# Optimization experiments

Measured on AMD Instinct MI355X. Metric: run time of the kernel, lower is better.

The kernel has to match this reference:

```python
import jax, jax.numpy as jnp
import numpy as np

N_NODES = 1024
CHANNELS = [1, 64, 128]
DENSE = [196608, 256]
SAMPLE_NUMBER = 50


def _glorot(key, shape):
    fan_in, fan_out = shape[0], shape[-1]
    s = jnp.sqrt(6.0 / (fan_in + fan_out))
    return jax.random.uniform(key, shape, jnp.float32, -s, s)


def setup_inputs() -> dict:
    key = jax.random.key(0)
    ks = jax.random.split(key, 20)
    T, B = 16, 64
    inp = {
        "xs_seq": jax.random.normal(ks[0], (T, B, N_NODES, CHANNELS[0]), jnp.float32),
        "adj": jax.random.uniform(ks[1], (N_NODES, N_NODES), jnp.float32) / N_NODES,
    }
    # GCGRU params per layer: gates z, r, candidate n over concat([x, h])
    ki = 2
    for li in range(len(CHANNELS) - 1):
        cin, cout = CHANNELS[li], CHANNELS[li + 1]
        for g in ("z", "r", "n"):
            inp[f"W{g}{li}"] = _glorot(ks[ki], (cin + cout, cout)); ki += 1
            inp[f"b{g}{li}"] = jnp.zeros((cout,), jnp.float32)
    inp["W_mu"] = _glorot(ks[ki], (DENSE[0], DENSE[1])); ki += 1
    inp["b_mu"] = jnp.zeros((DENSE[1],), jnp.float32)
    inp["W_lv"] = _glorot(ks[ki], (DENSE[0], DENSE[1])); ki += 1
    inp["b_lv"] = jnp.zeros((DENSE[1],), jnp.float32)
    return inp


def _gcgru(xs, adj, Wz, bz, Wr, br, Wn, bn, cout):
    # xs: [T, B, N, cin]; graph-conv GRU over time via scan
    T, B, N, _ = xs.shape
    h0 = jnp.zeros((B, N, cout), xs.dtype)

    def gconv(a, x, W, b):  # adj @ x @ W + b
        return jnp.einsum("ij,bjc,cd->bid", a, x, W) + b

    def step(h, x):
        xh = jnp.concatenate([x, h], axis=-1)
        z = jax.nn.sigmoid(gconv(adj, xh, Wz, bz))
        r = jax.nn.sigmoid(gconv(adj, xh, Wr, br))
        xrh = jnp.concatenate([x, r * h], axis=-1)
        n = jnp.tanh(gconv(adj, xrh, Wn, bn))
        h_new = (1.0 - z) * h + z * n
        return h_new, h_new

    _, hs = jax.lax.scan(step, h0, xs)
    return hs  # [T, B, N, cout]


def _forward(xs_seq, adj, Wz0, bz0, Wr0, br0, Wn0, bn0,
             Wz1, bz1, Wr1, br1, Wn1, bn1, W_mu, b_mu, W_lv, b_lv, eps):
    h1 = _gcgru(xs_seq, adj, Wz0, bz0, Wr0, br0, Wn0, bn0, CHANNELS[1])
    h2 = _gcgru(h1, adj, Wz1, bz1, Wr1, br1, Wn1, bn1, CHANNELS[2])
    xs = jnp.concatenate([h1[-1], h2[-1]], axis=2)  # [B, N, C1+C2]
    B = xs.shape[0]
    xs = xs.reshape(B, -1)  # [B, N*(C1+C2)]
    mu = jax.nn.sigmoid(xs @ W_mu + b_mu)
    logvar = jax.nn.sigmoid(xs @ W_lv + b_lv)
    std = jnp.exp(0.5 * logvar)
    z = mu + eps * std
    return z, mu, logvar


def reference(xs_seq, adj, Wz0, bz0, Wr0, br0, Wn0, bn0,
              Wz1, bz1, Wr1, br1, Wn1, bn1, W_mu, b_mu, W_lv, b_lv):
    B = xs_seq.shape[1]
    ekey = jax.random.fold_in(jax.random.key(0), 1234)
    eps = jax.random.normal(ekey, (SAMPLE_NUMBER, B, DENSE[1]), jnp.float32).mean(0)
    return _forward(xs_seq, adj, Wz0, bz0, Wr0, br0, Wn0, bn0,
                    Wz1, bz1, Wr1, br1, Wn1, bn1, W_mu, b_mu, W_lv, b_lv, eps)
```

## Files before the change

### kernel.cpp

```cpp
#include <hip/hip_runtime.h>
#include <math.h>

#define EPS_MODE 0

typedef unsigned short u16;
typedef short bf16x8 __attribute__((ext_vector_type(8)));
typedef float f32x4 __attribute__((ext_vector_type(4)));
typedef u16 u16x4 __attribute__((ext_vector_type(4)));
typedef u16 u16x8 __attribute__((ext_vector_type(8)));

static constexpr int T = 16;
static constexpr size_t MF = 1u << 20;
static constexpr int DKCH = 256;
static constexpr int DKCHUNK = 196608 / DKCH;

__device__ __forceinline__ u16 f2bf(float f) {
  unsigned u = __float_as_uint(f);
  unsigned r = (u + 0x7fffu + ((u >> 16) & 1u)) >> 16;
  return (u16)r;
}
__device__ __forceinline__ float bf2f(u16 h) {
  return __uint_as_float(((unsigned)h) << 16);
}
__device__ __forceinline__ void gload16(const void* g, void* l) {
  __builtin_amdgcn_global_load_lds(
      (const __attribute__((address_space(1))) void*)g,
      (__attribute__((address_space(3))) void*)l, 16, 0, 0);
}
__device__ __forceinline__ float sigm(float x) { return 1.f / (1.f + expf(-x)); }

__global__ __launch_bounds__(256) void cast_bf16(const float* __restrict__ in,
                                                 u16* __restrict__ out, int n) {
  int i = (blockIdx.x * 256 + threadIdx.x) * 4;
  if (i < n) {
    float4 v = *reinterpret_cast<const float4*>(&in[i]);
    out[i + 0] = f2bf(v.x); out[i + 1] = f2bf(v.y);
    out[i + 2] = f2bf(v.z); out[i + 3] = f2bf(v.w);
  }
}

__global__ __launch_bounds__(256) void prep_wt(const float* __restrict__ Wz0, const float* __restrict__ Wr0,
                                               const float* __restrict__ Wn0, const float* __restrict__ Wz1,
                                               const float* __restrict__ Wr1, const float* __restrict__ Wn1,
                                               u16* __restrict__ WzrT0, u16* __restrict__ WnT0,
                                               u16* __restrict__ WzrT1, u16* __restrict__ WnT1) {
  int seg = blockIdx.y;
  int idx = blockIdx.x * 256 + threadIdx.x;
  if (seg == 0) {
    if (idx < 128 * 64) {
      int j = idx >> 6, k = idx & 63;
      float v = (j < 64) ? Wz0[(k + 1) * 64 + j] : Wr0[(k + 1) * 64 + (j - 64)];
      WzrT0[idx] = f2bf(v);
    }
  } else if (seg == 1) {
    if (idx < 64 * 64) {
      int j = idx >> 6, k = idx & 63;
      WnT0[idx] = f2bf(Wn0[(k + 1) * 64 + j]);
    }
  } else if (seg == 2) {
    if (idx < 256 * 192) {
      int j = idx / 192, k = idx % 192;
      float v = (j < 128) ? Wz1[k * 128 + j] : Wr1[k * 128 + (j - 128)];
      WzrT1[idx] = f2bf(v);
    }
  } else {
    if (idx < 128 * 192) {
      int j = idx / 192, k = idx % 192;
      WnT1[idx] = f2bf(Wn1[k * 128 + j]);
    }
  }
}

template <int EPI, int LOGC, int MFR>
__global__ __launch_bounds__(256) void adj_mfma(const u16* __restrict__ A,
                                                const u16* __restrict__ BT,
                                                void* __restrict__ OUT) {
  constexpr int MT = MFR * 32;
  __shared__ __align__(16) char lds[(MFR + 4) * 4096];
  int tid = threadIdx.x;
  int w = tid >> 6, lane = tid & 63;
  int row0 = blockIdx.y * MT, col0 = blockIdx.x * 128;
  int wm = w >> 1, wn = w & 1;
  f32x4 acc[MFR][4] = {};
  for (int k0 = 0; k0 < 1024; k0 += 64) {
#pragma unroll
    for (int q = 0; q < MFR; ++q) {
      int row = q * 32 + w * 8 + (lane >> 3);
      gload16(A + (size_t)(row0 + row) * 1024 + k0 + (lane & 7) * 8,
              lds + q * 4096 + w * 1024);
    }
#pragma unroll
    for (int q = 0; q < 4; ++q) {
      int row = q * 32 + w * 8 + (lane >> 3);
      gload16(BT + (size_t)(col0 + row) * 1024 + k0 + (lane & 7) * 8,
              lds + MFR * 4096 + q * 4096 + w * 1024);
    }
    __syncthreads();
#pragma unroll
    for (int kk = 0; kk < 2; ++kk) {
      bf16x8 a[MFR], bb[4];
#pragma unroll
      for (int m = 0; m < MFR; ++m)
        a[m] = *(const bf16x8*)(lds + (wm * (MFR * 16) + m * 16 + (lane & 15)) * 128 + kk * 64 + (lane >> 4) * 16);
#pragma unroll
      for (int n = 0; n < 4; ++n)
        bb[n] = *(const bf16x8*)(lds + MFR * 4096 + (wn * 64 + n * 16 + (lane & 15)) * 128 + kk * 64 + (lane >> 4) * 16);
#pragma unroll
      for (int m = 0; m < MFR; ++m)
#pragma unroll
        for (int n = 0; n < 4; ++n)
          acc[m][n] = __builtin_amdgcn_mfma_f32_16x16x32_bf16(a[m], bb[n], acc[m][n], 0, 0, 0);
    }
    __syncthreads();
  }
  if (EPI == 1) {
    float* O = (float*)OUT;
#pragma unroll
    for (int m = 0; m < MFR; ++m)
#pragma unroll
      for (int n = 0; n < 4; ++n) {
        int col = col0 + wn * 64 + n * 16 + (lane & 15);
        int t = col >> 6, bbx = col & 63;
        int row = row0 + wm * (MFR * 16) + m * 16 + ((lane >> 4) << 2);
        *(float4*)&O[((size_t)t << 16) + ((size_t)bbx << 10) + row] = *(float4*)&acc[m][n];
      }
  } else {
    u16* O = (u16*)OUT;
    constexpr int C = 1 << LOGC;
#pragma unroll
    for (int m = 0; m < MFR; ++m)
#pragma unroll
      for (int n = 0; n < 4; ++n) {
        int col = col0 + wn * 64 + n * 16 + (lane & 15);
        int bbx = col >> LOGC, c = col & (C - 1);
#pragma unroll
        for (int j = 0; j < 4; ++j) {
          int row = row0 + wm * (MFR * 16) + m * 16 + ((lane >> 4) << 2) + j;
          O[(((size_t)bbx << 10) + row) * C + c] = f2bf(acc[m][n][j]);
        }
      }
  }
}

template <int C, int RK1, int MFR>
__global__ __launch_bounds__(256) void adj_ngate(
    const u16* __restrict__ A, const u16* __restrict__ BT,
    const u16* __restrict__ WnT, const float* __restrict__ bias,
    const float* __restrict__ axv, const float* __restrict__ wx,
    const u16* __restrict__ AH1, const u16* __restrict__ zT,
    u16* __restrict__ hT) {
  constexpr int LOGC = (C == 64) ? 6 : 7;
  constexpr int KW = (C == 64) ? 64 : 192;
  constexpr int KKAN = C / 32;
  constexpr int MT = MFR * 32;
  constexpr int STG = (MFR + 4) * 4096;
  constexpr int ANBYTES = MT * 136 * 2;
  constexpr int LDSZ = STG > ANBYTES ? STG : ANBYTES;
  __shared__ __align__(16) char lds[LDSZ];
  int tid = threadIdx.x;
  int w = tid >> 6, lane = tid & 63;
  int row0 = blockIdx.y * MT, col0 = blockIdx.x * 128;
  int wm = w >> 1, wn = w & 1;
  f32x4 acc[MFR][4] = {};
  for (int k0 = 0; k0 < 1024; k0 += 64) {
#pragma unroll
    for (int q = 0; q < MFR; ++q) {
      int row = q * 32 + w * 8 + (lane >> 3);
      gload16(A + (size_t)(row0 + row) * 1024 + k0 + (lane & 7) * 8,
              lds + q * 4096 + w * 1024);
    }
#pragma unroll
    for (int q = 0; q < 4; ++q) {
      int row = q * 32 + w * 8 + (lane >> 3);
      gload16(BT + (size_t)(col0 + row) * 1024 + k0 + (lane & 7) * 8,
              lds + MFR * 4096 + q * 4096 + w * 1024);
    }
    __syncthreads();
#pragma unroll
    for (int kk = 0; kk < 2; ++kk) {
      bf16x8 a[MFR], bb[4];
#pragma unroll
      for (int m = 0; m < MFR; ++m)
        a[m] = *(const bf16x8*)(lds + (wm * (MFR * 16) + m * 16 + (lane & 15)) * 128 + kk * 64 + (lane >> 4) * 16);
#pragma unroll
      for (int n = 0; n < 4; ++n)
        bb[n] = *(const bf16x8*)(lds + MFR * 4096 + (wn * 64 + n * 16 + (lane & 15)) * 128 + kk * 64 + (lane >> 4) * 16);
#pragma unroll
      for (int m = 0; m < MFR; ++m)
#pragma unroll
        for (int n = 0; n < 4; ++n)
          acc[m][n] = __builtin_amdgcn_mfma_f32_16x16x32_bf16(a[m], bb[n], acc[m][n], 0, 0, 0);
    }
    __syncthreads();
  }
  u16* ANt = (u16*)lds;
#pragma unroll
  for (int m = 0; m < MFR; ++m)
#pragma unroll
    for (int n = 0; n < 4; ++n) {
      int cl = wn * 64 + n * 16 + (lane & 15);
      int rl = wm * (MFR * 16) + m * 16 + ((lane >> 4) << 2);
#pragma unroll
      for (int j = 0; j < 4; ++j)
        ANt[(rl + j) * 136 + cl] = f2bf(acc[m][n][j]);
    }
  __syncthreads();
  int wrow = w >> 1, half = w & 1;
  int arow0 = wrow * (MFR * 16);
  int b0 = col0 >> LOGC;
  int out0 = (C == 64) ? 0 : half * 64;
  int kbase = (C == 64) ? half * 64 : 0;
  int b_eff = (C == 64) ? (b0 + half) : b0;
  constexpr int WOFF = (C == 64) ? 0 : 64;
  f32x4 acc2[MFR][4] = {};
#pragma unroll
  for (int kk = 0; kk < KKAN; ++kk) {
    bf16x8 a[MFR], bb[4];
    int ka = kbase + kk * 32 + (lane >> 4) * 8;
#pragma unroll
    for (int m = 0; m < MFR; ++m)
      a[m] = *(const bf16x8*)&ANt[(arow0 + m * 16 + (lane & 15)) * 136 + ka];
#pragma unroll
    for (int n = 0; n < 4; ++n)
      bb[n] = *(const bf16x8*)&WnT[(size_t)(out0 + n * 16 + (lane & 15)) * KW + WOFF + kk * 32 + (lane >> 4) * 8];
#pragma unroll
    for (int m = 0; m < MFR; ++m)
#pragma unroll
      for (int n = 0; n < 4; ++n)
        acc2[m][n] = __builtin_amdgcn_mfma_f32_16x16x32_bf16(a[m], bb[n], acc2[m][n], 0, 0, 0);
  }
  if (C == 128) {
#pragma unroll
    for (int kk = 0; kk < 2; ++kk) {
      bf16x8 a[MFR], bb[4];
#pragma unroll
      for (int m = 0; m < MFR; ++m)
        a[m] = *(const bf16x8*)&AH1[(((size_t)b0 << 10) + row0 + arow0 + m * 16 + (lane & 15)) * 64 + kk * 32 + (lane >> 4) * 8];
#pragma unroll
      for (int n = 0; n < 4; ++n)
        bb[n] = *(const bf16x8*)&WnT[(size_t)(out0 + n * 16 + (lane & 15)) * 192 + kk * 32 + (lane >> 4) * 8];
#pragma unroll
      for (int m = 0; m < MFR; ++m)
#pragma unroll
        for (int n = 0; n < 4; ++n)
          acc2[m][n] = __builtin_amdgcn_mfma_f32_16x16x32_bf16(a[m], bb[n], acc2[m][n], 0, 0, 0);
    }
  }
#pragma unroll
  for (int m = 0; m < MFR; ++m) {
    float ax4[4];
    if (RK1) {
      float4 v = *(const float4*)&axv[((size_t)b_eff << 10) + row0 + arow0 + m * 16 + ((lane >> 4) << 2)];
      ax4[0] = v.x; ax4[1] = v.y; ax4[2] = v.z; ax4[3] = v.w;
    }
#pragma unroll
    for (int n = 0; n < 4; ++n) {
      int cp = out0 + n * 16 + (lane & 15);
      int grow = arow0 + m * 16 + ((lane >> 4) << 2);
      size_t idx = (((size_t)b_eff << LOGC) + cp) * 1024 + row0 + grow;
      u16x4 zv = *(const u16x4*)&zT[idx];
      u16x4 hv = *(const u16x4*)&hT[idx];
      u16x4 pk;
#pragma unroll
      for (int j = 0; j < 4; ++j) {
        float g = acc2[m][n][j] + bias[cp];
        if (RK1) g += ax4[j] * wx[cp];
        float nv = tanhf(g);
        float z = bf2f(zv[j]), ho = bf2f(hv[j]);
        pk[j] = f2bf((1.f - z) * ho + z * nv);
      }
      *(u16x4*)&hT[idx] = pk;
    }
  }
}

template <int WM, int WN, int C, int NK1, int NK, int RK1>
__global__ __launch_bounds__(256) void gate_zr(
    const u16* __restrict__ A1, const u16* __restrict__ A2,
    const u16* __restrict__ WT, const float* __restrict__ bz,
    const float* __restrict__ br, const float* __restrict__ axv,
    const float* __restrict__ wxz, const float* __restrict__ wxr,
    const u16* __restrict__ hT, u16* __restrict__ zTo, u16* __restrict__ rhTo) {
  constexpr int MT = WM * 64, NT = WN * 64, K = NK * 64;
  constexpr int NB = 1024 / MT;
  __shared__ __align__(16) char lds[MT * 128 + NT * 128];
  int tid = threadIdx.x;
  int w = tid >> 6, lane = tid & 63;
  int by = blockIdx.x;
  int b = by / NB, n0 = (by % NB) * MT;
  size_t row0 = ((size_t)b << 10) + n0;
  int wm = w / WN, wn = w % WN;
  f32x4 acc[4][4] = {};
  for (int s = 0; s < NK; ++s) {
    const u16* As; int astr, koff;
    if (s < NK1) { As = A1; astr = 64; koff = s * 64; }
    else         { As = A2; astr = 128; koff = (s - NK1) * 64; }
#pragma unroll
    for (int q = 0; q < MT / 32; ++q) {
      int row = q * 32 + w * 8 + (lane >> 3);
      gload16(As + (row0 + row) * astr + koff + (lane & 7) * 8,
              lds + q * 4096 + w * 1024);
    }
#pragma unroll
    for (int q = 0; q < NT / 32; ++q) {
      int row = q * 32 + w * 8 + (lane >> 3);
      gload16(WT + (size_t)row * K + s * 64 + (lane & 7) * 8,
              lds + MT * 128 + q * 4096 + w * 1024);
    }
    __syncthreads();
#pragma unroll
    for (int kk = 0; kk < 2; ++kk) {
      bf16x8 a[4], bb[4];
#pragma unroll
      for (int m = 0; m < 4; ++m)
        a[m] = *(const bf16x8*)(lds + (wm * 64 + m * 16 + (lane & 15)) * 128 + kk * 64 + (lane >> 4) * 16);
#pragma unroll
      for (int n = 0; n < 4; ++n)
        bb[n] = *(const bf16x8*)(lds + MT * 128 + (wn * 64 + n * 16 + (lane & 15)) * 128 + kk * 64 + (lane >> 4) * 16);
#pragma unroll
      for (int m = 0; m < 4; ++m)
#pragma unroll
        for (int n = 0; n < 4; ++n)
          acc[m][n] = __builtin_amdgcn_mfma_f32_16x16x32_bf16(a[m], bb[n], acc[m][n], 0, 0, 0);
    }
    __syncthreads();
  }
#pragma unroll
  for (int m = 0; m < 4; ++m) {
    float ax4[4];
    if (RK1) {
      float4 v = *(const float4*)&axv[row0 + wm * 64 + m * 16 + ((lane >> 4) << 2)];
      ax4[0] = v.x; ax4[1] = v.y; ax4[2] = v.z; ax4[3] = v.w;
    }
#pragma unroll
    for (int n = 0; n < 4; ++n) {
      int cp = wn * 64 + n * 16 + (lane & 15);
      bool iz = cp < C;
      int c = iz ? cp : cp - C;
      int rl = wm * 64 + m * 16 + ((lane >> 4) << 2);
      size_t idx = (((size_t)b * C + c) << 10) + n0 + rl;
      u16x4 hv;
      if (!iz) hv = *(const u16x4*)&hT[idx];
      u16x4 pk;
#pragma unroll
      for (int j = 0; j < 4; ++j) {
        float g = acc[m][n][j] + (iz ? bz : br)[c];
        if (RK1) g += ax4[j] * (iz ? wxz : wxr)[c];
        float sg = sigm(g);
        pk[j] = iz ? f2bf(sg) : f2bf(sg * bf2f(hv[j]));
      }
      *(u16x4*)&(iz ? zTo : rhTo)[idx] = pk;
    }
  }
}

__global__ __launch_bounds__(256) void ah1_zr(
    const u16* __restrict__ adjB, const u16* __restrict__ h1T,
    const u16* __restrict__ AH2, const u16* __restrict__ h2T,
    const u16* __restrict__ WzrT1, const float* __restrict__ bz1, const float* __restrict__ br1,
    const u16* __restrict__ WzrT0, const float* __restrict__ bz0, const float* __restrict__ br0,
    const float* __restrict__ AXt1, const float* __restrict__ wz0x, const float* __restrict__ wr0x,
    u16* __restrict__ AH1, u16* __restrict__ z1T, u16* __restrict__ rh1T,
    u16* __restrict__ z0T, u16* __restrict__ rh0T, int do_zr0) {
  __shared__ __align__(16) char lds[24576];
  int tid = threadIdx.x, w = tid >> 6, lane = tid & 63;
  int row0 = blockIdx.y * 64, col0 = blockIdx.x * 128;
  int b0 = col0 >> 6;
  int wm = w >> 1, wn = w & 1;
  f32x4 acc[2][4] = {};
  for (int k0 = 0; k0 < 1024; k0 += 64) {
#pragma unroll
    for (int q = 0; q < 2; ++q) {
      int row = q * 32 + w * 8 + (lane >> 3);
      gload16(adjB + (size_t)(row0 + row) * 1024 + k0 + (lane & 7) * 8,
              lds + q * 4096 + w * 1024);
    }
#pragma unroll
    for (int q = 0; q < 4; ++q) {
      int row = q * 32 + w * 8 + (lane >> 3);
      gload16(h1T + (size_t)(col0 + row) * 1024 + k0 + (lane & 7) * 8,
              lds + 8192 + q * 4096 + w * 1024);
    }
    __syncthreads();
#pragma unroll
    for (int kk = 0; kk < 2; ++kk) {
      bf16x8 a[2], bb[4];
#pragma unroll
      for (int m = 0; m < 2; ++m)
        a[m] = *(const bf16x8*)(lds + (wm * 32 + m * 16 + (lane & 15)) * 128 + kk * 64 + (lane >> 4) * 16);
#pragma unroll
      for (int n = 0; n < 4; ++n)
        bb[n] = *(const bf16x8*)(lds + 8192 + (wn * 64 + n * 16 + (lane & 15)) * 128 + kk * 64 + (lane >> 4) * 16);
#pragma unroll
      for (int m = 0; m < 2; ++m)
#pragma unroll
        for (int n = 0; n < 4; ++n)
          acc[m][n] = __builtin_amdgcn_mfma_f32_16x16x32_bf16(a[m], bb[n], acc[m][n], 0, 0, 0);
    }
    __syncthreads();
  }
  u16* ANt = (u16*)lds;
#pragma unroll
  for (int m = 0; m < 2; ++m)
#pragma unroll
    for (int n = 0; n < 4; ++n) {
      int col = wn * 64 + n * 16 + (lane & 15);
      int bl = col >> 6, c = col & 63;
      int rl = wm * 32 + m * 16 + ((lane >> 4) << 2);
#pragma unroll
      for (int j = 0; j < 4; ++j) {
        u16 v = f2bf(acc[m][n][j]);
        AH1[(((size_t)(b0 + bl) << 10) + row0 + rl + j) * 64 + c] = v;
        ANt[(bl * 64 + rl + j) * 72 + c] = v;
      }
    }
  __syncthreads();
  int b = b0 + wm;
#pragma unroll
  for (int hz = 0; hz < 2; ++hz) {
    f32x4 g1[4][4] = {};
#pragma unroll
    for (int kk = 0; kk < 2; ++kk) {
      bf16x8 a[4], bb[4];
#pragma unroll
      for (int m = 0; m < 4; ++m)
        a[m] = *(const bf16x8*)&ANt[(wm * 64 + m * 16 + (lane & 15)) * 72 + kk * 32 + (lane >> 4) * 8];
#pragma unroll
      for (int n = 0; n < 4; ++n) {
        int out = hz * 128 + wn * 64 + n * 16 + (lane & 15);
        bb[n] = *(const bf16x8*)&WzrT1[(size_t)out * 192 + kk * 32 + (lane >> 4) * 8];
      }
#pragma unroll
      for (int m = 0; m < 4; ++m)
#pragma unroll
        for (int n = 0; n < 4; ++n)
          g1[m][n] = __builtin_amdgcn_mfma_f32_16x16x32_bf16(a[m], bb[n], g1[m][n], 0, 0, 0);
    }
#pragma unroll
    for (int kk = 0; kk < 4; ++kk) {
      bf16x8 a[4], bb[4];
#pragma unroll
      for (int m = 0; m < 4; ++m) {
        int gn = row0 + m * 16 + (lane & 15);
        a[m] = *(const bf16x8*)&AH2[(((size_t)b << 10) + gn) * 128 + kk * 32 + (lane >> 4) * 8];
      }
#pragma unroll
      for (int n = 0; n < 4; ++n) {
        int out = hz * 128 + wn * 64 + n * 16 + (lane & 15);
        bb[n] = *(const bf16x8*)&WzrT1[(size_t)out * 192 + 64 + kk * 32 + (lane >> 4) * 8];
      }
#pragma unroll
      for (int m = 0; m < 4; ++m)
#pragma unroll
        for (int n = 0; n < 4; ++n)
          g1[m][n] = __builtin_amdgcn_mfma_f32_16x16x32_bf16(a[m], bb[n], g1[m][n], 0, 0, 0);
    }
#pragma unroll
    for (int m = 0; m < 4; ++m)
#pragma unroll
      for (int n = 0; n < 4; ++n) {
        int outq = hz * 128 + wn * 64 + n * 16 + (lane & 15);
        bool iz = outq < 128;
        int c = iz ? outq : outq - 128;
        int gr = m * 16 + ((lane >> 4) << 2);
        size_t idx = (((size_t)b * 128 + c) << 10) + row0 + gr;
        u16x4 hv;
        if (!iz) hv = *(const u16x4*)&h2T[idx];
        u16x4 pk;
#pragma unroll
        for (int j = 0; j < 4; ++j) {
          float g = g1[m][n][j] + (iz ? bz1 : br1)[c];
          float sg = sigm(g);
          pk[j] = iz ? f2bf(sg) : f2bf(sg * bf2f(hv[j]));
        }
        *(u16x4*)&(iz ? z1T : rh1T)[idx] = pk;
      }
  }
  if (do_zr0) {
    f32x4 g0[4][4] = {};
#pragma unroll
    for (int kk = 0; kk < 2; ++kk) {
      bf16x8 a[4], bb[4];
#pragma unroll
      for (int m = 0; m < 4; ++m)
        a[m] = *(const bf16x8*)&ANt[(wm * 64 + m * 16 + (lane & 15)) * 72 + kk * 32 + (lane >> 4) * 8];
#pragma unroll
      for (int n = 0; n < 4; ++n) {
        int out = wn * 64 + n * 16 + (lane & 15);
        bb[n] = *(const bf16x8*)&WzrT0[(size_t)out * 64 + kk * 32 + (lane >> 4) * 8];
      }
#pragma unroll
      for (int m = 0; m < 4; ++m)
#pragma unroll
        for (int n = 0; n < 4; ++n)
          g0[m][n] = __builtin_amdgcn_mfma_f32_16x16x32_bf16(a[m], bb[n], g0[m][n], 0, 0, 0);
    }
#pragma unroll
    for (int m = 0; m < 4; ++m) {
      int gr0 = m * 16 + ((lane >> 4) << 2);
      float4 av = *(const float4*)&AXt1[((size_t)b << 10) + row0 + gr0];
      float ax4[4] = {av.x, av.y, av.z, av.w};
#pragma unroll
      for (int n = 0; n < 4; ++n) {
        int out = wn * 64 + n * 16 + (lane & 15);
        bool iz = out < 64;
        int c = out & 63;
        size_t idx = (((size_t)b * 64 + c) << 10) + row0 + gr0;
        u16x4 hv;
        if (!iz) hv = *(const u16x4*)&h1T[idx];
        u16x4 pk;
#pragma unroll
        for (int j = 0; j < 4; ++j) {
          float g = g0[m][n][j] + (iz ? bz0 : br0)[c] + ax4[j] * (iz ? wz0x : wr0x)[c];
          float sg = sigm(g);
          pk[j] = iz ? f2bf(sg) : f2bf(sg * bf2f(hv[j]));
        }
        *(u16x4*)&(iz ? z0T : rh0T)[idx] = pk;
      }
    }
  }
}

__global__ __launch_bounds__(256) void transpose_x(const u16* __restrict__ h1T,
                                                   const u16* __restrict__ h2T,
                                                   u16* __restrict__ X) {
  int b = blockIdx.x;
  int n0 = blockIdx.y * 128;
  __shared__ u16 tile[192][136];
  int tid = threadIdx.x;
#pragma unroll
  for (int i = 0; i < 12; ++i) {
    int id = tid + i * 256;
    int c = id >> 4, g = id & 15;
    u16x8 v;
    if (c < 64) v = *(const u16x8*)&h1T[(((size_t)b << 6) + c) * 1024 + n0 + g * 8];
    else        v = *(const u16x8*)&h2T[(((size_t)b << 7) + (c - 64)) * 1024 + n0 + g * 8];
    *(u16x8*)&tile[c][g * 8] = v;
  }
  __syncthreads();
#pragma unroll
  for (int i = 0; i < 12; ++i) {
    int id = tid + i * 256;
    int n = id / 24, g = id % 24;
    u16x8 v;
#pragma unroll
    for (int j = 0; j < 8; ++j) v[j] = tile[g * 8 + j][n];
    *(u16x8*)&X[(size_t)b * 196608 + (size_t)(n0 + n) * 192 + g * 8] = v;
  }
}

__global__ __launch_bounds__(256) void dense_mfma3(const u16* __restrict__ X,
                                                   const float* __restrict__ Wmu,
                                                   const float* __restrict__ Wlv,
                                                   float* __restrict__ P) {
  __shared__ __align__(16) char lds[8192 + 128 * 70 * 2];
  u16* Bs = (u16*)(lds + 8192);
  int tid = threadIdx.x, w = tid >> 6, lane = tid & 63;
  int o0 = blockIdx.x * 128;
  int ch = blockIdx.y, mat = blockIdx.z;
  const float* W = mat ? Wlv : Wmu;
  int kb = ch * DKCHUNK;
  int oL = tid & 63;
  f32x4 acc[4][2] = {};
  for (int s = 0; s < DKCHUNK / 64; ++s) {
    int kg = kb + s * 64;
#pragma unroll
    for (int q = 0; q < 2; ++q) {
      int row = q * 32 + w * 8 + (lane >> 3);
      gload16(X + (size_t)row * 196608 + kg + (lane & 7) * 8,
              lds + q * 4096 + w * 1024);
    }
#pragma unroll
    for (int og = 0; og < 2; ++og) {
      int o = og * 64 + oL;
      float v[16];
#pragma unroll
      for (int kk = 0; kk < 16; ++kk)
        v[kk] = W[(size_t)(kg + w * 16 + kk) * 256 + o0 + o];
      u16x8 p0, p1;
#pragma unroll
      for (int j = 0; j < 8; ++j) p0[j] = f2bf(v[j]);
#pragma unroll
      for (int j = 0; j < 8; ++j) p1[j] = f2bf(v[8 + j]);
      *(u16x8*)&Bs[o * 70 + w * 16] = p0;
      *(u16x8*)&Bs[o * 70 + w * 16 + 8] = p1;
    }
    __syncthreads();
#pragma unroll
    for (int kk = 0; kk < 2; ++kk) {
      bf16x8 a[4], bb[2];
#pragma unroll
      for (int m = 0; m < 4; ++m)
        a[m] = *(const bf16x8*)(lds + (m * 16 + (lane & 15)) * 128 + kk * 64 + (lane >> 4) * 16);
#pragma unroll
      for (int n = 0; n < 2; ++n) {
        int o = w * 32 + n * 16 + (lane & 15);
        bb[n] = *(const bf16x8*)&Bs[o * 70 + kk * 32 + (lane >> 4) * 8];
      }
#pragma unroll
      for (int m = 0; m < 4; ++m)
#pragma unroll
        for (int n = 0; n < 2; ++n)
          acc[m][n] = __builtin_amdgcn_mfma_f32_16x16x32_bf16(a[m], bb[n], acc[m][n], 0, 0, 0);
    }
    __syncthreads();
  }
#pragma unroll
  for (int m = 0; m < 4; ++m)
#pragma unroll
    for (int n = 0; n < 2; ++n) {
      int o = o0 + w * 32 + n * 16 + (lane & 15);
#pragma unroll
      for (int j = 0; j < 4; ++j) {
        int row = m * 16 + ((lane >> 4) << 2) + j;
        P[(((size_t)mat * DKCH + ch) * 64 + row) * 256 + o] = acc[m][n][j];
      }
    }
}

__device__ __forceinline__ unsigned rotl32(unsigned v, int s) {
  return (v << s) | (v >> (32 - s));
}
__device__ void threefry(unsigned k0, unsigned k1, unsigned x0, unsigned x1,
                         unsigned& o0, unsigned& o1) {
  unsigned ks2 = k0 ^ k1 ^ 0x1BD11BDAu;
  unsigned a = x0 + k0, b = x1 + k1;
#define TF_RND(rot) { a += b; b = rotl32(b, rot); b ^= a; }
  TF_RND(13) TF_RND(15) TF_RND(26) TF_RND(6)
  a += k1; b += ks2 + 1u;
  TF_RND(17) TF_RND(29) TF_RND(16) TF_RND(24)
  a += ks2; b += k0 + 2u;
  TF_RND(13) TF_RND(15) TF_RND(26) TF_RND(6)
  a += k0; b += k1 + 3u;
  TF_RND(17) TF_RND(29) TF_RND(16) TF_RND(24)
  a += k1; b += ks2 + 4u;
  TF_RND(13) TF_RND(15) TF_RND(26) TF_RND(6)
  a += ks2; b += k0 + 5u;
#undef TF_RND
  o0 = a; o1 = b;
}

__device__ float u32_to_normal(unsigned bits) {
  unsigned fb = (bits >> 9) | 0x3F800000u;
  float f = __uint_as_float(fb) - 1.0f;
  const float lo = -0.99999994f;
  float u = f * 2.0f + lo;
  u = fmaxf(lo, u);
  float w = -log1pf(-u * u);
  float p;
  if (w < 5.0f) {
    w -= 2.5f;
    p = 2.81022636e-08f;
    p = fmaf(p, w, 3.43273939e-07f);
    p = fmaf(p, w, -3.5233877e-06f);
    p = fmaf(p, w, -4.39150654e-06f);
    p = fmaf(p, w, 0.00021858087f);
    p = fmaf(p, w, -0.00125372503f);
    p = fmaf(p, w, -0.00417768164f);
    p = fmaf(p, w, 0.246640727f);
    p = fmaf(p, w, 1.50140941f);
  } else {
    w = sqrtf(w) - 3.0f;
    p = -0.000200214257f;
    p = fmaf(p, w, 0.000100950558f);
    p = fmaf(p, w, 0.00134934322f);
    p = fmaf(p, w, -0.00367342844f);
    p = fmaf(p, w, 0.00573950773f);
    p = fmaf(p, w, -0.0076224613f);
    p = fmaf(p, w, 0.00943887047f);
    p = fmaf(p, w, 1.00167406f);
    p = fmaf(p, w, 2.83297682f);
  }
  return 1.41421354f * (p * u);
}

__global__ __launch_bounds__(256) void eps_kernel(float* __restrict__ eps) {
  int b = blockIdx.x;
  int o = threadIdx.x;
  unsigned k0, k1;
  threefry(0u, 0u, 0u, 1234u, k0, k1);
  float s = 0.f;
  for (int smp = 0; smp < 50; ++smp) {
    unsigned idx = ((unsigned)smp * 64u + (unsigned)b) * 256u + (unsigned)o;
    unsigned o0, o1, bits;
#if EPS_MODE == 0
    threefry(k0, k1, 0u, idx, o0, o1);
    bits = o0 ^ o1;
#else
    unsigned pp = idx % 409600u, half = idx / 409600u;
    threefry(k0, k1, pp, pp + 409600u, o0, o1);
    bits = half ? o1 : o0;
#endif
    s += u32_to_normal(bits);
  }
  eps[b * 256 + o] = s / 50.0f;
}

__global__ __launch_bounds__(256) void final_kernel(const float* __restrict__ P,
                                                    const float* __restrict__ bmu,
                                                    const float* __restrict__ blv,
                                                    const float* __restrict__ eps,
                                                    float* __restrict__ out) {
  int b = blockIdx.x, o = threadIdx.x;
  float smu = 0.f, slv = 0.f;
  for (int ch = 0; ch < DKCH; ++ch) {
    smu += P[(((size_t)0 * DKCH + ch) * 64 + b) * 256 + o];
    slv += P[(((size_t)1 * DKCH + ch) * 64 + b) * 256 + o];
  }
  float mu = sigm(smu + bmu[o]);
  float lv = sigm(slv + blv[o]);
  float z = mu + eps[b * 256 + o] * expf(0.5f * lv);
  out[b * 256 + o] = z;
  out[16384 + b * 256 + o] = mu;
  out[32768 + b * 256 + o] = lv;
}

extern "C" void kernel_launch(void* const* d_in, const int* in_sizes, int n_in,
                              void* d_out, int out_size, void* d_ws, size_t ws_size,
                              hipStream_t stream) {
  (void)in_sizes; (void)n_in; (void)out_size; (void)ws_size;
  const float* xs  = (const float*)d_in[0];
  const float* adj = (const float*)d_in[1];
  const float* Wz0 = (const float*)d_in[2];  const float* bz0 = (const float*)d_in[3];
  const float* Wr0 = (const float*)d_in[4];  const float* br0 = (const float*)d_in[5];
  const float* Wn0 = (const float*)d_in[6];  const float* bn0 = (const float*)d_in[7];
  const float* Wz1 = (const float*)d_in[8];  const float* bz1 = (const float*)d_in[9];
  const float* Wr1 = (const float*)d_in[10]; const float* br1 = (const float*)d_in[11];
  const float* Wn1 = (const float*)d_in[12]; const float* bn1 = (const float*)d_in[13];
  const float* Wmu = (const float*)d_in[14]; const float* bmu = (const float*)d_in[15];
  const float* Wlv = (const float*)d_in[16]; const float* blv = (const float*)d_in[17];

  float* ws = (float*)d_ws;
  u16*  adjB  = (u16*)(ws);
  u16*  xsB   = (u16*)(ws + MF / 2);
  float* AXv  = ws + 1 * MF;
  u16*  h1T   = (u16*)(ws + 2 * MF);
  u16*  h2T   = (u16*)(ws + 4 * MF);
  u16*  z0T   = (u16*)(ws + 8 * MF);
  u16*  z1T   = (u16*)(ws + 10 * MF);
  u16*  rh0T  = (u16*)(ws + 14 * MF);
  u16*  rh1T  = (u16*)(ws + 16 * MF);
  u16*  AH1   = (u16*)(ws + 20 * MF);
  u16*  AH2   = (u16*)(ws + 22 * MF);
  u16*  WTb   = (u16*)(ws + 26 * MF);
  u16*  X     = (u16*)(ws + 8 * MF);
  float* P    = ws + 16 * MF;
  float* EPS  = ws + 24 * MF;

  u16* WzrT0 = WTb;
  u16* WnT0  = WTb + 8192;
  u16* WzrT1 = WTb + 12288;
  u16* WnT1  = WTb + 61440;

  hipMemsetAsync(ws + 2 * MF, 0, 6 * MF * sizeof(float), stream);
  hipMemsetAsync(ws + 20 * MF, 0, 6 * MF * sizeof(float), stream);

  cast_bf16<<<1024, 256, 0, stream>>>(adj, adjB, 1 << 20);
  cast_bf16<<<1024, 256, 0, stream>>>(xs, xsB, 1 << 20);
  prep_wt<<<dim3(192, 4), 256, 0, stream>>>(Wz0, Wr0, Wn0, Wz1, Wr1, Wn1,
                                            WzrT0, WnT0, WzrT1, WnT1);

  adj_mfma<1, 0, 4><<<dim3(8, 8), 256, 0, stream>>>(adjB, xsB, AXv);

  gate_zr<2, 2, 64, 1, 1, 1><<<512, 256, 0, stream>>>(
      AH1, nullptr, WzrT0, bz0, br0, AXv, Wz0, Wr0, h1T, z0T, rh0T);

  for (int t = 0; t < T; ++t) {
    const float* AXt = AXv + (size_t)t * 65536;
    const float* AXn = AXv + (size_t)((t + 1 < T) ? t + 1 : t) * 65536;
    adj_ngate<64, 1, 2><<<dim3(32, 16), 256, 0, stream>>>(
        adjB, rh0T, WnT0, bn0, AXt, Wn0, nullptr, z0T, h1T);
    ah1_zr<<<dim3(32, 16), 256, 0, stream>>>(
        adjB, h1T, AH2, h2T, WzrT1, bz1, br1, WzrT0, bz0, br0,
        AXn, Wz0, Wr0, AH1, z1T, rh1T, z0T, rh0T, (t + 1 < T) ? 1 : 0);
    adj_ngate<128, 0, 4><<<dim3(64, 8), 256, 0, stream>>>(
        adjB, rh1T, WnT1, bn1, nullptr, nullptr, AH1, z1T, h2T);
    if (t + 1 < T)
      adj_mfma<0, 7, 4><<<dim3(64, 8), 256, 0, stream>>>(adjB, h2T, AH2);
  }

  transpose_x<<<dim3(64, 8), 256, 0, stream>>>(h1T, h2T, X);
  dense_mfma3<<<dim3(2, DKCH, 2), 256, 0, stream>>>(X, Wmu, Wlv, P);
  eps_kernel<<<64, 256, 0, stream>>>(EPS);
  final_kernel<<<64, 256, 0, stream>>>(P, bmu, blv, EPS, (float*)d_out);
}
```

Measured before the change: 2.784 ms.

## Fuse next-step layer-0 n-gate with layer-1 adj matmul into one launch

Turns the adj_mfma and adj_ngate bodies into device functions and adds a combo_tail kernel. Its first 512 blocks compute the layer-1 A·h2 product and its remaining 512 blocks run the layer-0 n-gate for the next timestep. This reschedules the time loop so layer 0 runs one step ahead, which cuts one launch per step and lets two independent GEMMs fill the GPU at the same time. It also doubles the dense K-split count (DKCH 256→512) and moves the EPS buffer, presumably to make room for the larger partial-sum buffer, at the cost of more partial sums to reduce.

New measurement: 2.757 ms. No clear change (-1.0%).

```diff
diff --git a/kernel.cpp b/kernel.cpp
--- a/kernel.cpp
+++ b/kernel.cpp
@@ -11,7 +11,7 @@
 
 static constexpr int T = 16;
 static constexpr size_t MF = 1u << 20;
-static constexpr int DKCH = 256;
+static constexpr int DKCH = 512;
 static constexpr int DKCHUNK = 196608 / DKCH;
 
 __device__ __forceinline__ u16 f2bf(float f) {
@@ -72,14 +72,14 @@
 }
 
 template <int EPI, int LOGC, int MFR>
-__global__ __launch_bounds__(256) void adj_mfma(const u16* __restrict__ A,
-                                                const u16* __restrict__ BT,
-                                                void* __restrict__ OUT) {
+__device__ __forceinline__ void dev_adj_mfma(int bx, int by, char* lds,
+                                             const u16* __restrict__ A,
+                                             const u16* __restrict__ BT,
+                                             void* __restrict__ OUT) {
   constexpr int MT = MFR * 32;
-  __shared__ __align__(16) char lds[(MFR + 4) * 4096];
   int tid = threadIdx.x;
   int w = tid >> 6, lane = tid & 63;
-  int row0 = blockIdx.y * MT, col0 = blockIdx.x * 128;
+  int row0 = by * MT, col0 = bx * 128;
   int wm = w >> 1, wn = w & 1;
   f32x4 acc[MFR][4] = {};
   for (int k0 = 0; k0 < 1024; k0 += 64) {
@@ -142,8 +142,17 @@
   }
 }
 
+template <int EPI, int LOGC, int MFR>
+__global__ __launch_bounds__(256) void adj_mfma(const u16* __restrict__ A,
+                                                const u16* __restrict__ BT,
+                                                void* __restrict__ OUT) {
+  __shared__ __align__(16) char lds[(MFR + 4) * 4096];
+  dev_adj_mfma<EPI, LOGC, MFR>(blockIdx.x, blockIdx.y, lds, A, BT, OUT);
+}
+
 template <int C, int RK1, int MFR>
-__global__ __launch_bounds__(256) void adj_ngate(
+__device__ __forceinline__ void dev_adj_ngate(
+    int bx, int by, char* lds,
     const u16* __restrict__ A, const u16* __restrict__ BT,
     const u16* __restrict__ WnT, const float* __restrict__ bias,
     const float* __restrict__ axv, const float* __restrict__ wx,
@@ -153,13 +162,9 @@
   constexpr int KW = (C == 64) ? 64 : 192;
   constexpr int KKAN = C / 32;
   constexpr int MT = MFR * 32;
-  constexpr int STG = (MFR + 4) * 4096;
-  constexpr int ANBYTES = MT * 136 * 2;
-  constexpr int LDSZ = STG > ANBYTES ? STG : ANBYTES;
-  __shared__ __align__(16) char lds[LDSZ];
   int tid = threadIdx.x;
   int w = tid >> 6, lane = tid & 63;
-  int row0 = blockIdx.y * MT, col0 = blockIdx.x * 128;
+  int row0 = by * MT, col0 = bx * 128;
   int wm = w >> 1, wn = w & 1;
   f32x4 acc[MFR][4] = {};
   for (int k0 = 0; k0 < 1024; k0 += 64) {
@@ -271,6 +276,38 @@
       }
       *(u16x4*)&hT[idx] = pk;
     }
+  }
+}
+
+template <int C, int RK1, int MFR>
+__global__ __launch_bounds__(256) void adj_ngate(
+    const u16* __restrict__ A, const u16* __restrict__ BT,
+    const u16* __restrict__ WnT, const float* __restrict__ bias,
+    const float* __restrict__ axv, const float* __restrict__ wx,
+    const u16* __restrict__ AH1, const u16* __restrict__ zT,
+    u16* __restrict__ hT) {
+  constexpr int MT = MFR * 32;
+  constexpr int STG = (MFR + 4) * 4096;
+  constexpr int ANB = MT * 136 * 2;
+  constexpr int LDSZ = STG > ANB ? STG : ANB;
+  __shared__ __align__(16) char lds[LDSZ];
+  dev_adj_ngate<C, RK1, MFR>(blockIdx.x, blockIdx.y, lds, A, BT, WnT, bias, axv, wx,
+                             AH1, zT, hT);
+}
+
+__global__ __launch_bounds__(256) void combo_tail(
+    const u16* __restrict__ adjB, const u16* __restrict__ h2T, u16* __restrict__ AH2,
+    const u16* __restrict__ rh0T, const u16* __restrict__ WnT0, const float* __restrict__ bn0,
+    const float* __restrict__ AXt1, const float* __restrict__ Wn0,
+    const u16* __restrict__ z0T, u16* __restrict__ h1T) {
+  __shared__ __align__(16) char lds[32768];
+  int bid = blockIdx.x;
+  if (bid < 512) {
+    dev_adj_mfma<0, 7, 4>(bid & 63, bid >> 6, lds, adjB, h2T, AH2);
+  } else {
+    int b2 = bid - 512;
+    dev_adj_ngate<64, 1, 2>(b2 & 31, b2 >> 5, lds, adjB, rh0T, WnT0, bn0,
+                            AXt1, Wn0, nullptr, z0T, h1T);
   }
 }
 
@@ -745,7 +782,7 @@
   u16*  WTb   = (u16*)(ws + 26 * MF);
   u16*  X     = (u16*)(ws + 8 * MF);
   float* P    = ws + 16 * MF;
-  float* EPS  = ws + 24 * MF;
+  float* EPS  = ws + 33 * MF;
 
   u16* WzrT0 = WTb;
   u16* WnT0  = WTb + 8192;
@@ -764,19 +801,19 @@
 
   gate_zr<2, 2, 64, 1, 1, 1><<<512, 256, 0, stream>>>(
       AH1, nullptr, WzrT0, bz0, br0, AXv, Wz0, Wr0, h1T, z0T, rh0T);
+  adj_ngate<64, 1, 2><<<dim3(32, 16), 256, 0, stream>>>(
+      adjB, rh0T, WnT0, bn0, AXv, Wn0, nullptr, z0T, h1T);
 
   for (int t = 0; t < T; ++t) {
-    const float* AXt = AXv + (size_t)t * 65536;
     const float* AXn = AXv + (size_t)((t + 1 < T) ? t + 1 : t) * 65536;
-    adj_ngate<64, 1, 2><<<dim3(32, 16), 256, 0, stream>>>(
-        adjB, rh0T, WnT0, bn0, AXt, Wn0, nullptr, z0T, h1T);
     ah1_zr<<<dim3(32, 16), 256, 0, stream>>>(
         adjB, h1T, AH2, h2T, WzrT1, bz1, br1, WzrT0, bz0, br0,
         AXn, Wz0, Wr0, AH1, z1T, rh1T, z0T, rh0T, (t + 1 < T) ? 1 : 0);
     adj_ngate<128, 0, 4><<<dim3(64, 8), 256, 0, stream>>>(
         adjB, rh1T, WnT1, bn1, nullptr, nullptr, AH1, z1T, h2T);
     if (t + 1 < T)
-      adj_mfma<0, 7, 4><<<dim3(64, 8), 256, 0, stream>>>(adjB, h2T, AH2);
+      combo_tail<<<1024, 256, 0, stream>>>(adjB, h2T, AH2, rh0T, WnT0, bn0,
+                                           AXn, Wn0, z0T, h1T);
   }
 
   transpose_x<<<dim3(64, 8), 256, 0, stream>>>(h1T, h2T, X);
```
